# Kernel optimization log

Measured on AMD Instinct MI355X. Metric: run time of the kernel, lower is better.

The kernel has to match this reference:

```python
import jax, jax.numpy as jnp
import numpy as np

B, H, W, CIN, C, L = 2, 512, 512, 64, 64, 4
TAU = 1.0


def _conv3x3(x, w):
    # NHWC input, HWIO kernel, SAME zero padding, stride 1 (SignalConv2D corr=True)
    return jax.lax.conv_general_dilated(
        x, w, window_strides=(1, 1), padding='SAME',
        dimension_numbers=('NHWC', 'HWIO', 'NHWC'))


def setup_inputs() -> dict:
    key = jax.random.key(0)
    ks = jax.random.split(key, 10)
    return {
        'x0': jax.random.normal(ks[0], (B, H, W, CIN), jnp.float32),
        'spa_mask': jax.random.uniform(ks[1], (B, H, W, 1), jnp.float32),
        'gumbel_u': jax.random.uniform(ks[2], (1, L, 2, C), jnp.float32),
        'ch_mask': jax.random.uniform(ks[3], (1, L, 2, C), jnp.float32),
        'w0': jax.random.normal(ks[4], (3, 3, CIN, C), jnp.float32) * 0.05,
        'w1': jax.random.normal(ks[5], (3, 3, C, C), jnp.float32) * 0.05,
        'w2': jax.random.normal(ks[6], (3, 3, C, C), jnp.float32) * 0.05,
        'w3': jax.random.normal(ks[7], (3, 3, C, C), jnp.float32) * 0.05,
        'w_collect': jax.random.normal(ks[8], (L * C, C), jnp.float32) * 0.05,
        'b_collect': jnp.zeros((C,), jnp.float32),
    }


def reference(x0, spa_mask, gumbel_u, ch_mask, w0, w1, w2, w3, w_collect, b_collect):
    # Gumbel-softmax channel routing mask over the {dense, sparse} axis (axis=2)
    g = -jnp.log(-jnp.log(jnp.clip(gumbel_u, 1e-10, 1.0)))
    ch = jax.nn.softmax((ch_mask + g) / TAU, axis=2)  # (1, L, 2, C)

    ws = [w0, w1, w2, w3]
    out_feats = []
    fea = x0
    for i in range(L):
        cd = ch[:, i, 0, :][:, None, None, :]  # dense-channel mask  (1,1,1,C)
        cs = ch[:, i, 1, :][:, None, None, :]  # sparse-channel mask (1,1,1,C)
        if i == 0:
            fea = _conv3x3(fea, ws[0])
            fea = fea * cs * spa_mask + fea * cd
        else:
            cdp = ch[:, i - 1, 0, :][:, None, None, :]
            csp = ch[:, i - 1, 1, :][:, None, None, :]
            fea_d = _conv3x3(fea * cdp, ws[i])
            fea_s = _conv3x3(fea * csp, ws[i])
            fea = (fea_d * cs * spa_mask + fea_d * cd
                   + fea_s * cs * spa_mask + fea_s * cd * spa_mask)
        fea = jax.nn.relu(fea)
        out_feats.append(fea)

    cat = jnp.concatenate(out_feats, axis=-1)  # (B, H, W, L*C)
    # 1x1 stride-1 Conv2DTranspose == pointwise linear + bias
    out = jnp.einsum('bhwi,io->bhwo', cat, w_collect) + b_collect
    return out, ch
```

## Files before the change

### kernel.cpp

```cpp
#include <hip/hip_runtime.h>
#include <hip/hip_fp16.h>

#define BB 2
#define HH 512
#define WW 512
#define CC 64
#define PW 514

typedef _Float16 f16;
typedef _Float16 f16x8 __attribute__((ext_vector_type(8)));
typedef float f32x4 __attribute__((ext_vector_type(4)));

static __device__ __forceinline__ f16x8 zero_f16x8() {
    f16x8 z = {(f16)0,(f16)0,(f16)0,(f16)0,(f16)0,(f16)0,(f16)0,(f16)0};
    return z;
}

static __device__ __forceinline__ f16x8 cvt_pair(f32x4 a, f32x4 b) {
    f16x8 o;
    o[0]=(f16)a[0]; o[1]=(f16)a[1]; o[2]=(f16)a[2]; o[3]=(f16)a[3];
    o[4]=(f16)b[0]; o[5]=(f16)b[1]; o[6]=(f16)b[2]; o[7]=(f16)b[3];
    return o;
}

__global__ void k_prep_ch(const float* __restrict__ gum, const float* __restrict__ chm,
                          float* __restrict__ ws_ch, float* __restrict__ out_ch) {
    int t = threadIdx.x;
    int l = t >> 6, c = t & 63;
    float u0 = gum[(l*2+0)*64+c], u1 = gum[(l*2+1)*64+c];
    u0 = fminf(fmaxf(u0, 1e-10f), 1.0f);
    u1 = fminf(fmaxf(u1, 1e-10f), 1.0f);
    float a0 = chm[(l*2+0)*64+c] - logf(-logf(u0));
    float a1 = chm[(l*2+1)*64+c] - logf(-logf(u1));
    float m = fmaxf(a0, a1);
    float e0 = expf(a0-m), e1 = expf(a1-m);
    float s = e0 + e1;
    float c0 = e0/s, c1 = e1/s;
    ws_ch[(l*2+0)*64+c] = c0;  ws_ch[(l*2+1)*64+c] = c1;
    out_ch[(l*2+0)*64+c] = c0; out_ch[(l*2+1)*64+c] = c1;
}

__global__ void k_pack(const float* __restrict__ w0, const float* __restrict__ w1,
                       const float* __restrict__ w2, const float* __restrict__ w3,
                       const float* __restrict__ wc, const float* __restrict__ ch,
                       f16* __restrict__ bpk0, f16* __restrict__ bpkL, f16* __restrict__ wcpk) {
    int idx = blockIdx.x * 256 + threadIdx.x;
    if (idx < 36864) {
        int j = idx & 7, lane = (idx>>3)&63, nb = (idx>>9)&3, kb = idx>>11;
        int k = kb*32 + (lane>>4)*8 + j;
        int tap = k>>6, ci = k&63;
        int co = nb*16 + (lane&15);
        bpk0[idx] = (f16)w0[(tap*64+ci)*64+co];
    } else if (idx < 36864 + 221184) {
        int i2 = idx - 36864;
        int l = i2 / 73728;
        int r = i2 % 73728;
        int j = r&7, lane=(r>>3)&63, nb=(r>>9)&7, kb=r>>12;
        int k = kb*32 + (lane>>4)*8 + j;
        int tap = k>>6, ci = k&63;
        int copr = nb*16 + (lane&15);
        int co = copr & 63;
        const float* w = (l==0)? w1 : (l==1)? w2 : w3;
        float scale = (copr < 64) ? ch[(l*2+0)*64+ci] : ch[(l*2+1)*64+ci];
        bpkL[i2] = (f16)(w[(tap*64+ci)*64+co] * scale);
    } else if (idx < 36864 + 221184 + 16384) {
        int i3 = idx - (36864 + 221184);
        int j=i3&7, lane=(i3>>3)&63, nb=(i3>>9)&3, kb=(i3>>11)&1, l=i3>>12;
        int k = kb*32 + (lane>>4)*8 + j;
        int n = nb*16 + (lane&15);
        wcpk[i3] = (f16)wc[(l*64+k)*64+n];
    }
}

__global__ void k_guard(f16* __restrict__ b1, f16* __restrict__ b2, f16* __restrict__ b3) {
    f16* buf = (blockIdx.y == 0) ? b1 : (blockIdx.y == 1) ? b2 : b3;
    int idx = blockIdx.x*256 + threadIdx.x;
    const int TOT = 2*2052*8;
    if (idx >= TOT) return;
    int c8 = idx & 7, g = idx >> 3;
    int b = g / 2052, r = g % 2052;
    int hp, wp;
    if      (r < 514)  { hp = 0;        wp = r; }
    else if (r < 1028) { hp = 513;      wp = r-514; }
    else if (r < 1540) { hp = r-1027;   wp = 0; }
    else               { hp = r-1539;   wp = 513; }
    *(f16x8*)(buf + ((size_t)(b*PW+hp)*PW + wp)*64 + c8*8) = zero_f16x8();
}

template<int MODE>
__global__ __launch_bounds__(256, 2) void k_conv(const void* __restrict__ in_, f16* __restrict__ out,
        const f16* __restrict__ bpk, const float* __restrict__ ch_l,
        const float* __restrict__ spa) {
    constexpr int NBT = (MODE==0) ? 4 : 8;
    constexpr int NF  = (MODE==0) ? 2 : 4;
    __shared__ f16 smem[4*136*64];
    const int bid = blockIdx.x;
    const int xcd = bid & 7;
    const int wt  = xcd & 3;
    const int b   = xcd >> 2;
    const int hb  = bid >> 3;
    const int h0 = hb*2;
    const int tid = threadIdx.x, lane = tid & 63, wid = tid >> 6;
    const int px0 = wt*128;
    const int sub  = lane & 7;
    const int srel = lane >> 3;
    const int cblk = sub ^ srel;

    if (MODE == 0) {
        const float* inF = (const float*)in_;
        #pragma unroll
        for (int half = 0; half < 2; ++half) {
            const int J0 = half ? 9 : 0;
            const int JN = half ? 8 : 9;
            f32x4 v0[9], v1[9];
            bool ok[9];
            int dst[9];
            #pragma unroll
            for (int t = 0; t < JN; ++t) {
                int j = (J0 + t)*4 + wid;
                int r = j / 17, i = j % 17;
                int s = i*8 + srel;
                int hin = h0 + r - 1;
                int win = px0 + s - 1;
                ok[t] = ((unsigned)hin < HH) && ((unsigned)win < WW);
                dst[t] = r*17408 + i*1024 + lane*16;
                if (ok[t]) {
                    const f32x4* p = (const f32x4*)(inF + (((size_t)(b*HH + hin)*WW + win)*CC + cblk*8));
                    v0[t] = p[0];
                    v1[t] = p[1];
                }
            }
            #pragma unroll
            for (int t = 0; t < JN; ++t) {
                f16x8 o = ok[t] ? cvt_pair(v0[t], v1[t]) : zero_f16x8();
                if ((J0 + t)*4 + wid < 68)
                    *(f16x8*)((char*)smem + dst[t]) = o;
            }
        }
        __syncthreads();
    } else {
        const f16* inH = (const f16*)in_;
        #pragma unroll
        for (int jj = 0; jj < 9; ++jj) {
            int j = jj*4 + wid;
            if (j < 34) {
                int r = j / 17, i = j % 17;
                int s = i*8 + srel;
                const f16* src = inH + ((size_t)(b*PW + h0 + r)*PW + (px0 + s))*64 + cblk*8;
                __builtin_amdgcn_global_load_lds(
                    (const __attribute__((address_space(1))) uint32_t*)src,
                    (__attribute__((address_space(3))) uint32_t*)
                        ((char*)smem + r*17408 + i*1024),
                    16, 0, 0);
            }
        }
        __syncthreads();
        #pragma unroll
        for (int jj = 0; jj < 9; ++jj) {
            int j = 34 + jj*4 + wid;
            if (j < 68) {
                int r = j / 17, i = j % 17;
                int s = i*8 + srel;
                const f16* src = inH + ((size_t)(b*PW + h0 + r)*PW + (px0 + s))*64 + cblk*8;
                __builtin_amdgcn_global_load_lds(
                    (const __attribute__((address_space(1))) uint32_t*)src,
                    (__attribute__((address_space(3))) uint32_t*)
                        ((char*)smem + r*17408 + i*1024),
                    16, 0, 0);
            }
        }
    }

    const int wr = wid >> 1, wn = wid & 1;
    const int lrow = lane & 15, q = lane >> 4;
    const char* smw = (const char*)smem + wr*17408;

    int sb[8][3], po[2][3];
    #pragma unroll
    for (int dxi = 0; dxi < 3; ++dxi) {
        int m7 = (lrow + dxi) & 7;
        po[0][dxi] = ((q)     ^ m7) * 16;
        po[1][dxi] = ((4 + q) ^ m7) * 16;
        #pragma unroll
        for (int mf = 0; mf < 8; ++mf)
            sb[mf][dxi] = (mf*16 + lrow + dxi) * 128;
    }

    f32x4 acc[8][NF];
    #pragma unroll
    for (int i=0;i<8;i++)
        #pragma unroll
        for (int j=0;j<NF;j++) { f32x4 z = {0.f,0.f,0.f,0.f}; acc[i][j] = z; }

    int nbIdx[4];
    nbIdx[0]=wn*2; nbIdx[1]=wn*2+1; nbIdx[2]=wn*2+4; nbIdx[3]=wn*2+5;

    const f16* blane = bpk + (size_t)lane*8;

    f16x8 acur[8], anxt[8], bcur[NF], bnxt[NF];
    #pragma unroll
    for (int nf=0; nf<NF; ++nf)
        bcur[nf] = *reinterpret_cast<const f16x8*>(blane + (size_t)nbIdx[nf]*512);
    #pragma unroll
    for (int mf=0; mf<8; ++mf)
        acur[mf] = *(const f16x8*)(smw + sb[mf][0] + po[0][0]);

    #pragma unroll
    for (int kb = 0; kb < 18; ++kb) {
        if (MODE == 1 && kb == 5) __syncthreads();
        if (kb < 17) {
            const int kn = kb + 1;
            const int rn = kn/6, dxin = (kn%6)/2, halfn = kn & 1;
            #pragma unroll
            for (int nf=0; nf<NF; ++nf)
                bnxt[nf] = *reinterpret_cast<const f16x8*>(blane + (size_t)(kn*NBT + nbIdx[nf])*512);
            #pragma unroll
            for (int mf=0; mf<8; ++mf)
                anxt[mf] = *(const f16x8*)(smw + rn*17408 + sb[mf][dxin] + po[halfn][dxin]);
        }
        __builtin_amdgcn_s_setprio(1);
        #pragma unroll
        for (int nf=0; nf<NF; ++nf) {
            #pragma unroll
            for (int mf=0; mf<8; ++mf)
                acc[mf][nf] = __builtin_amdgcn_mfma_f32_16x16x32_f16(acur[mf], bcur[nf], acc[mf][nf], 0,0,0);
        }
        __builtin_amdgcn_s_setprio(0);
        #pragma unroll
        for (int nf=0; nf<NF; ++nf) bcur[nf] = bnxt[nf];
        #pragma unroll
        for (int mf=0; mf<8; ++mf) acur[mf] = anxt[mf];
    }

    const float* cd = ch_l;
    const float* cs = ch_l + 64;
    const int h = h0 + wr;
    const size_t sparow = (size_t)(b*HH + h)*WW;
    const size_t outrow = (size_t)(b*PW + h + 1)*PW + 1;
    #pragma unroll
    for (int mf=0; mf<8; ++mf) {
        const int pixb = mf*16 + q*4;
        f32x4 sp4 = *(const f32x4*)(spa + sparow + px0 + pixb);
        float sp[4] = {sp4[0], sp4[1], sp4[2], sp4[3]};
        #pragma unroll
        for (int nf2=0; nf2<2; ++nf2) {
            int co = wn*32 + nf2*16 + lrow;
            float vcd = cd[co], vcs = cs[co];
            #pragma unroll
            for (int r=0; r<4; ++r) {
                float v;
                if (MODE==0) v = acc[mf][nf2][r] * (vcs*sp[r] + vcd);
                else         v = acc[mf][nf2][r] * (vcs*sp[r] + vcd) + acc[mf][nf2+2][r] * sp[r];
                v = fmaxf(v, 0.f);
                out[(outrow + px0 + pixb + r)*64 + co] = (f16)v;
            }
        }
    }
}

__global__ __launch_bounds__(256) void k_collect_all(
        const f16* __restrict__ f0, const f16* __restrict__ f1,
        const f16* __restrict__ f2, const f16* __restrict__ f3,
        const f16* __restrict__ wcpk, const float* __restrict__ bias,
        float* __restrict__ out) {
    const int wt = blockIdx.x, h = blockIdx.y, b = blockIdx.z;
    const int tid = threadIdx.x;
    const int lane = tid & 63, wid = tid >> 6;
    const int lrow = lane & 15, lk = (lane>>4)*8;
    const size_t inrow  = (size_t)(b*PW + h + 1)*PW + 1;
    const size_t outrow = (size_t)(b*HH + h)*WW;
    const int px0 = wt*256 + wid*64;

    const f16* feas[4] = {f0, f1, f2, f3};

    f32x4 acc[4][4];
    #pragma unroll
    for (int i=0;i<4;i++)
        #pragma unroll
        for (int j=0;j<4;j++) { f32x4 z = {0.f,0.f,0.f,0.f}; acc[i][j] = z; }

    #pragma unroll
    for (int kb=0; kb<8; ++kb) {
        const f16* fl = feas[kb>>1];
        f16x8 a[4];
        #pragma unroll
        for (int mf=0; mf<4; ++mf)
            a[mf] = *reinterpret_cast<const f16x8*>(fl + (inrow + px0 + mf*16 + lrow)*64 + (kb&1)*32 + lk);
        #pragma unroll
        for (int nf=0; nf<4; ++nf) {
            f16x8 bb = *reinterpret_cast<const f16x8*>(wcpk + ((size_t)(kb*4 + nf)*64 + lane)*8);
            #pragma unroll
            for (int mf=0; mf<4; ++mf)
                acc[mf][nf] = __builtin_amdgcn_mfma_f32_16x16x32_f16(bb, a[mf], acc[mf][nf], 0,0,0);
        }
    }
    const int q = lane >> 4;
    #pragma unroll
    for (int mf=0; mf<4; ++mf) {
        const int pix = px0 + mf*16 + lrow;
        float* orow = out + (outrow + pix)*CC;
        #pragma unroll
        for (int nf=0; nf<4; ++nf) {
            const int co0 = nf*16 + q*4;
            f32x4 b4 = *(const f32x4*)(bias + co0);
            *(f32x4*)(orow + co0) = acc[mf][nf] + b4;
        }
    }
}

template<bool FIRST>
__global__ __launch_bounds__(256) void k_collect(const f16* __restrict__ fea,
        const f16* __restrict__ wcpk_l, const float* __restrict__ bias,
        float* __restrict__ out) {
    const int wt = blockIdx.x, h = blockIdx.y, b = blockIdx.z;
    const int tid = threadIdx.x;
    const int lane = tid & 63, wid = tid >> 6;
    const int lrow = lane & 15, lk = (lane>>4)*8;
    const size_t inrow  = (size_t)(b*PW + h + 1)*PW + 1;
    const size_t outrow = (size_t)(b*HH + h)*WW;
    const int px0 = wt*64 + wid*16;

    f32x4 acc[4];
    #pragma unroll
    for (int j=0;j<4;j++) { f32x4 z = {0.f,0.f,0.f,0.f}; acc[j] = z; }

    #pragma unroll
    for (int kb=0; kb<2; ++kb) {
        f16x8 a = *reinterpret_cast<const f16x8*>(fea + (inrow + px0 + lrow)*64 + kb*32 + lk);
        #pragma unroll
        for (int nf=0; nf<4; ++nf) {
            f16x8 bb = *reinterpret_cast<const f16x8*>(wcpk_l + ((size_t)(kb*4 + nf)*64 + lane)*8);
            acc[nf] = __builtin_amdgcn_mfma_f32_16x16x32_f16(bb, a, acc[nf], 0,0,0);
        }
    }
    const int q = lane >> 4;
    const int pix = px0 + lrow;
    float* orow = out + (outrow + pix)*CC;
    #pragma unroll
    for (int nf=0; nf<4; ++nf) {
        const int co0 = nf*16 + q*4;
        f32x4 v = acc[nf];
        #pragma unroll
        for (int r=0;r<4;++r) {
            float x = v[r];
            if (FIRST) x += bias[co0+r];
            else       x += orow[co0+r];
            orow[co0+r] = x;
        }
    }
}

extern "C" void kernel_launch(void* const* d_in, const int* in_sizes, int n_in,
                              void* d_out, int out_size, void* d_ws, size_t ws_size,
                              hipStream_t stream) {
    const float* x0  = (const float*)d_in[0];
    const float* spa = (const float*)d_in[1];
    const float* gum = (const float*)d_in[2];
    const float* chm = (const float*)d_in[3];
    const float* w0  = (const float*)d_in[4];
    const float* w1  = (const float*)d_in[5];
    const float* w2  = (const float*)d_in[6];
    const float* w3  = (const float*)d_in[7];
    const float* wc  = (const float*)d_in[8];
    const float* bias= (const float*)d_in[9];
    float* out = (float*)d_out;

    char* ws = (char*)d_ws;
    const size_t WBASE = (1u<<20);
    const size_t FB = 67699712ull;
    const size_t NEED_A = WBASE + 4*FB;
    const size_t NEED_B = WBASE + 2*FB;
    if (ws_size < NEED_B) return;

    float* ws_ch = (float*)ws;
    f16* bpk0 = (f16*)(ws + 4096);
    f16* bpkL = (f16*)(ws + 4096 + 73728);
    f16* wcpk = (f16*)(ws + 4096 + 73728 + 442368);

    k_prep_ch<<<1, 256, 0, stream>>>(gum, chm, ws_ch, out + 33554432);
    k_pack<<<1072, 256, 0, stream>>>(w0, w1, w2, w3, wc, ws_ch, bpk0, bpkL, wcpk);

    dim3 gcv(2048, 1, 1);
    dim3 gca(2, 512, 2);
    dim3 gcf(8, 512, 2);
    dim3 ggd(129, 3, 1);

    if (ws_size >= NEED_A) {
        f16* R0 = (f16*)(ws + WBASE);
        f16* R1 = (f16*)(ws + WBASE + FB);
        f16* R2 = (f16*)(ws + WBASE + 2*FB);
        f16* R3 = (f16*)(ws + WBASE + 3*FB);
        k_guard<<<ggd, 256, 0, stream>>>(R1, R2, R3);
        k_conv<0><<<gcv, 256, 0, stream>>>(x0, R1, bpk0,          ws_ch + 0,   spa);
        k_conv<1><<<gcv, 256, 0, stream>>>(R1, R2, bpkL + 0,      ws_ch + 128, spa);
        k_conv<1><<<gcv, 256, 0, stream>>>(R2, R3, bpkL + 73728,  ws_ch + 256, spa);
        k_conv<1><<<gcv, 256, 0, stream>>>(R3, R0, bpkL + 147456, ws_ch + 384, spa);
        k_collect_all<<<gca, 256, 0, stream>>>(R1, R2, R3, R0, wcpk, bias, out);
    } else {
        f16* P0 = (f16*)(ws + WBASE);
        f16* P1 = (f16*)(ws + WBASE + FB);
        k_guard<<<ggd, 256, 0, stream>>>(P0, P1, P0);
        k_conv<0><<<gcv, 256, 0, stream>>>(x0, P1, bpk0,          ws_ch + 0,   spa);
        k_collect<true ><<<gcf, 256, 0, stream>>>(P1, wcpk + 0,     bias, out);
        k_conv<1><<<gcv, 256, 0, stream>>>(P1, P0, bpkL + 0,      ws_ch + 128, spa);
        k_collect<false><<<gcf, 256, 0, stream>>>(P0, wcpk + 4096,  bias, out);
        k_conv<1><<<gcv, 256, 0, stream>>>(P0, P1, bpkL + 73728,  ws_ch + 256, spa);
        k_collect<false><<<gcf, 256, 0, stream>>>(P1, wcpk + 8192,  bias, out);
        k_conv<1><<<gcv, 256, 0, stream>>>(P1, P0, bpkL + 147456, ws_ch + 384, spa);
        k_collect<false><<<gcf, 256, 0, stream>>>(P0, wcpk + 12288, bias, out);
    }
}
```

Baseline: 347.0 us.

## Merge setup kernels and retile collect with XCD-aware mapping and prefetch

Folds the channel-mask computation, weight packing and guard-border zeroing into a single setup kernel. The packing branch now recomputes the gumbel softmax inline instead of reading it from a prior kernel. This removes two launches and the serialization between them. The collect kernel now uses a 1D grid with XCD-interleaved block mapping, covers half as many pixels per wave, and register-prefetches the next K-block's activations so loads overlap the MFMAs. The cost is more blocks with less reuse of each weight fragment.

```diff
diff --git a/kernel.cpp b/kernel.cpp
--- a/kernel.cpp
+++ b/kernel.cpp
@@ -23,10 +23,8 @@
     return o;
 }
 
-__global__ void k_prep_ch(const float* __restrict__ gum, const float* __restrict__ chm,
-                          float* __restrict__ ws_ch, float* __restrict__ out_ch) {
-    int t = threadIdx.x;
-    int l = t >> 6, c = t & 63;
+static __device__ __forceinline__ float ch_scale(const float* gum, const float* chm,
+                                                 int l, int side, int c) {
     float u0 = gum[(l*2+0)*64+c], u1 = gum[(l*2+1)*64+c];
     u0 = fminf(fmaxf(u0, 1e-10f), 1.0f);
     u1 = fminf(fmaxf(u1, 1e-10f), 1.0f);
@@ -35,15 +33,17 @@
     float m = fmaxf(a0, a1);
     float e0 = expf(a0-m), e1 = expf(a1-m);
     float s = e0 + e1;
-    float c0 = e0/s, c1 = e1/s;
-    ws_ch[(l*2+0)*64+c] = c0;  ws_ch[(l*2+1)*64+c] = c1;
-    out_ch[(l*2+0)*64+c] = c0; out_ch[(l*2+1)*64+c] = c1;
-}
-
-__global__ void k_pack(const float* __restrict__ w0, const float* __restrict__ w1,
-                       const float* __restrict__ w2, const float* __restrict__ w3,
-                       const float* __restrict__ wc, const float* __restrict__ ch,
-                       f16* __restrict__ bpk0, f16* __restrict__ bpkL, f16* __restrict__ wcpk) {
+    return (side == 0) ? e0/s : e1/s;
+}
+
+__global__ void k_setup(const float* __restrict__ w0, const float* __restrict__ w1,
+                        const float* __restrict__ w2, const float* __restrict__ w3,
+                        const float* __restrict__ wc, const float* __restrict__ gum,
+                        const float* __restrict__ chm,
+                        float* __restrict__ ws_ch, float* __restrict__ out_ch,
+                        f16* __restrict__ bpk0, f16* __restrict__ bpkL,
+                        f16* __restrict__ wcpk,
+                        f16* __restrict__ g1, f16* __restrict__ g2, f16* __restrict__ g3) {
     int idx = blockIdx.x * 256 + threadIdx.x;
     if (idx < 36864) {
         int j = idx & 7, lane = (idx>>3)&63, nb = (idx>>9)&3, kb = idx>>11;
@@ -61,7 +61,7 @@
         int copr = nb*16 + (lane&15);
         int co = copr & 63;
         const float* w = (l==0)? w1 : (l==1)? w2 : w3;
-        float scale = (copr < 64) ? ch[(l*2+0)*64+ci] : ch[(l*2+1)*64+ci];
+        float scale = ch_scale(gum, chm, l, (copr < 64) ? 0 : 1, ci);
         bpkL[i2] = (f16)(w[(tap*64+ci)*64+co] * scale);
     } else if (idx < 36864 + 221184 + 16384) {
         int i3 = idx - (36864 + 221184);
@@ -69,22 +69,28 @@
         int k = kb*32 + (lane>>4)*8 + j;
         int n = nb*16 + (lane&15);
         wcpk[i3] = (f16)wc[(l*64+k)*64+n];
-    }
-}
-
-__global__ void k_guard(f16* __restrict__ b1, f16* __restrict__ b2, f16* __restrict__ b3) {
-    f16* buf = (blockIdx.y == 0) ? b1 : (blockIdx.y == 1) ? b2 : b3;
-    int idx = blockIdx.x*256 + threadIdx.x;
-    const int TOT = 2*2052*8;
-    if (idx >= TOT) return;
-    int c8 = idx & 7, g = idx >> 3;
-    int b = g / 2052, r = g % 2052;
-    int hp, wp;
-    if      (r < 514)  { hp = 0;        wp = r; }
-    else if (r < 1028) { hp = 513;      wp = r-514; }
-    else if (r < 1540) { hp = r-1027;   wp = 0; }
-    else               { hp = r-1539;   wp = 513; }
-    *(f16x8*)(buf + ((size_t)(b*PW+hp)*PW + wp)*64 + c8*8) = zero_f16x8();
+    } else if (idx < 36864 + 221184 + 16384 + 512) {
+        int t = idx - (36864 + 221184 + 16384);
+        int l = t >> 7, sc = t & 127;
+        int side = sc >> 6, c = sc & 63;
+        float v = ch_scale(gum, chm, l, side, c);
+        ws_ch[(l*2+side)*64+c] = v;
+        out_ch[(l*2+side)*64+c] = v;
+    } else {
+        int g = idx - (36864 + 221184 + 16384 + 512);
+        const int TOT = 2*2052*8;
+        if (g >= 3*TOT) return;
+        f16* buf = (g < TOT) ? g1 : (g < 2*TOT) ? g2 : g3;
+        int e = g % TOT;
+        int c8 = e & 7, gg = e >> 3;
+        int b = gg / 2052, r = gg % 2052;
+        int hp, wp;
+        if      (r < 514)  { hp = 0;        wp = r; }
+        else if (r < 1028) { hp = 513;      wp = r-514; }
+        else if (r < 1540) { hp = r-1027;   wp = 0; }
+        else               { hp = r-1539;   wp = 513; }
+        *(f16x8*)(buf + ((size_t)(b*PW+hp)*PW + wp)*64 + c8*8) = zero_f16x8();
+    }
 }
 
 template<int MODE>
@@ -263,40 +269,52 @@
         const f16* __restrict__ f2, const f16* __restrict__ f3,
         const f16* __restrict__ wcpk, const float* __restrict__ bias,
         float* __restrict__ out) {
-    const int wt = blockIdx.x, h = blockIdx.y, b = blockIdx.z;
+    const int bid = blockIdx.x;
+    const int xcd = bid & 7;
+    const int wtc = xcd & 3;
+    const int b   = xcd >> 2;
+    const int h   = bid >> 3;
     const int tid = threadIdx.x;
     const int lane = tid & 63, wid = tid >> 6;
     const int lrow = lane & 15, lk = (lane>>4)*8;
     const size_t inrow  = (size_t)(b*PW + h + 1)*PW + 1;
     const size_t outrow = (size_t)(b*HH + h)*WW;
-    const int px0 = wt*256 + wid*64;
+    const int px0 = wtc*128 + wid*32;
 
     const f16* feas[4] = {f0, f1, f2, f3};
 
-    f32x4 acc[4][4];
-    #pragma unroll
-    for (int i=0;i<4;i++)
+    f32x4 acc[2][4];
+    #pragma unroll
+    for (int i=0;i<2;i++)
         #pragma unroll
         for (int j=0;j<4;j++) { f32x4 z = {0.f,0.f,0.f,0.f}; acc[i][j] = z; }
 
+    f16x8 a_cur[2], a_nxt[2];
+    #pragma unroll
+    for (int mf=0; mf<2; ++mf)
+        a_cur[mf] = *reinterpret_cast<const f16x8*>(f0 + (inrow + px0 + mf*16 + lrow)*64 + lk);
+
     #pragma unroll
     for (int kb=0; kb<8; ++kb) {
-        const f16* fl = feas[kb>>1];
-        f16x8 a[4];
-        #pragma unroll
-        for (int mf=0; mf<4; ++mf)
-            a[mf] = *reinterpret_cast<const f16x8*>(fl + (inrow + px0 + mf*16 + lrow)*64 + (kb&1)*32 + lk);
+        if (kb < 7) {
+            const f16* fl = feas[(kb+1)>>1];
+            #pragma unroll
+            for (int mf=0; mf<2; ++mf)
+                a_nxt[mf] = *reinterpret_cast<const f16x8*>(fl + (inrow + px0 + mf*16 + lrow)*64 + ((kb+1)&1)*32 + lk);
+        }
         #pragma unroll
         for (int nf=0; nf<4; ++nf) {
             f16x8 bb = *reinterpret_cast<const f16x8*>(wcpk + ((size_t)(kb*4 + nf)*64 + lane)*8);
             #pragma unroll
-            for (int mf=0; mf<4; ++mf)
-                acc[mf][nf] = __builtin_amdgcn_mfma_f32_16x16x32_f16(bb, a[mf], acc[mf][nf], 0,0,0);
-        }
+            for (int mf=0; mf<2; ++mf)
+                acc[mf][nf] = __builtin_amdgcn_mfma_f32_16x16x32_f16(bb, a_cur[mf], acc[mf][nf], 0,0,0);
+        }
+        #pragma unroll
+        for (int mf=0; mf<2; ++mf) a_cur[mf] = a_nxt[mf];
     }
     const int q = lane >> 4;
     #pragma unroll
-    for (int mf=0; mf<4; ++mf) {
+    for (int mf=0; mf<2; ++mf) {
         const int pix = px0 + mf*16 + lrow;
         float* orow = out + (outrow + pix)*CC;
         #pragma unroll
@@ -377,29 +395,27 @@
     f16* bpkL = (f16*)(ws + 4096 + 73728);
     f16* wcpk = (f16*)(ws + 4096 + 73728 + 442368);
 
-    k_prep_ch<<<1, 256, 0, stream>>>(gum, chm, ws_ch, out + 33554432);
-    k_pack<<<1072, 256, 0, stream>>>(w0, w1, w2, w3, wc, ws_ch, bpk0, bpkL, wcpk);
-
     dim3 gcv(2048, 1, 1);
-    dim3 gca(2, 512, 2);
     dim3 gcf(8, 512, 2);
-    dim3 ggd(129, 3, 1);
+    const int SETUP_GRID = (36864 + 221184 + 16384 + 512 + 3*32832 + 255) / 256;
 
     if (ws_size >= NEED_A) {
         f16* R0 = (f16*)(ws + WBASE);
         f16* R1 = (f16*)(ws + WBASE + FB);
         f16* R2 = (f16*)(ws + WBASE + 2*FB);
         f16* R3 = (f16*)(ws + WBASE + 3*FB);
-        k_guard<<<ggd, 256, 0, stream>>>(R1, R2, R3);
+        k_setup<<<SETUP_GRID, 256, 0, stream>>>(w0, w1, w2, w3, wc, gum, chm,
+                ws_ch, out + 33554432, bpk0, bpkL, wcpk, R1, R2, R3);
         k_conv<0><<<gcv, 256, 0, stream>>>(x0, R1, bpk0,          ws_ch + 0,   spa);
         k_conv<1><<<gcv, 256, 0, stream>>>(R1, R2, bpkL + 0,      ws_ch + 128, spa);
         k_conv<1><<<gcv, 256, 0, stream>>>(R2, R3, bpkL + 73728,  ws_ch + 256, spa);
         k_conv<1><<<gcv, 256, 0, stream>>>(R3, R0, bpkL + 147456, ws_ch + 384, spa);
-        k_collect_all<<<gca, 256, 0, stream>>>(R1, R2, R3, R0, wcpk, bias, out);
+        k_collect_all<<<4096, 256, 0, stream>>>(R1, R2, R3, R0, wcpk, bias, out);
     } else {
         f16* P0 = (f16*)(ws + WBASE);
         f16* P1 = (f16*)(ws + WBASE + FB);
-        k_guard<<<ggd, 256, 0, stream>>>(P0, P1, P0);
+        k_setup<<<SETUP_GRID, 256, 0, stream>>>(w0, w1, w2, w3, wc, gum, chm,
+                ws_ch, out + 33554432, bpk0, bpkL, wcpk, P0, P1, P0);
         k_conv<0><<<gcv, 256, 0, stream>>>(x0, P1, bpk0,          ws_ch + 0,   spa);
         k_collect<true ><<<gcf, 256, 0, stream>>>(P1, wcpk + 0,     bias, out);
         k_conv<1><<<gcv, 256, 0, stream>>>(P1, P0, bpkL + 0,      ws_ch + 128, spa);
```

New measurement: 351.7 us. About the same (+1.3%).
